# Optimization experiments

Hardware: AMD Instinct MI355X
Metric: run time of the kernel (lower is better)

Reference implementation:

```python
import jax, jax.numpy as jnp
import numpy as np

H = 4      # n_heads
HD = 32    # head_dim
D = 128    # pair channels = H*HD
S = 384    # sequence length
EPS = 1e-5


def setup_inputs() -> dict:
    key = jax.random.key(0)
    ks = jax.random.split(key, 8)
    return {
        "x": jax.random.normal(ks[0], (1, S, S, D), dtype=jnp.float32),
        "attn_mask": jnp.zeros((1, 1, 1, S), dtype=jnp.float32),
        "ln_w": jax.random.uniform(ks[1], (D,), dtype=jnp.float32),
        "ln_b": jax.random.normal(ks[2], (D,), dtype=jnp.float32) * 0.02,
        "bias_w": jax.random.normal(ks[3], (H, D), dtype=jnp.float32) * 0.02,
        "qkv_w": jax.random.normal(ks[4], (3 * H * HD, D), dtype=jnp.float32) * 0.02,
        "g_w": jax.random.normal(ks[5], (H * HD, D), dtype=jnp.float32) * 0.02,
        "o_w": jax.random.normal(ks[6], (D, H * HD), dtype=jnp.float32) * 0.02,
    }


def reference(x, attn_mask, ln_w, ln_b, bias_w, qkv_w, g_w, o_w):
    # x: [1, S, S, D]; ending=False -> no permute
    xs = x[0]  # [S, S, D]; first S = batch of rows, second S = attended axis
    mu = jnp.mean(xs, axis=-1, keepdims=True)
    var = jnp.mean(jnp.square(xs - mu), axis=-1, keepdims=True)
    ln = (xs - mu) * jax.lax.rsqrt(var + EPS) * ln_w + ln_b  # [S, S, D]

    # triangle bias: D -> H, shaped [1, H, S, S], broadcast over row-batch
    bias = jnp.einsum('ijd,hd->hij', ln, bias_w)  # [H, S, S]

    # fused qkv projection, split heads
    qkv = jnp.einsum('bsd,ed->bse', ln, qkv_w)  # [S, S, 3*H*HD]
    q, k, v = jnp.split(qkv, 3, axis=-1)
    def heads(t):
        return t.reshape(S, S, H, HD).transpose(0, 2, 1, 3)  # [S, H, S, HD]
    q, k, v = heads(q), heads(k), heads(v)

    scale = 1.0 / jnp.sqrt(jnp.float32(HD))
    scores = jnp.einsum('bhqd,bhkd->bhqk', q, k) * scale  # [S, H, S, S]
    scores = scores + bias[None] + attn_mask  # attn_mask broadcasts [1,1,1,S]
    attn = jax.nn.softmax(scores, axis=-1)
    o = jnp.einsum('bhqk,bhkd->bhqd', attn, v)  # [S, H, S, HD]
    o = o.transpose(0, 2, 1, 3).reshape(S, S, H * HD)  # concat heads

    g = jnp.einsum('bsd,ed->bse', ln, g_w)  # [S, S, H*HD]
    o = o * jax.nn.sigmoid(g)
    out = jnp.einsum('bse,de->bsd', o, o_w)  # [S, S, D]
    return out[None]  # [1, S, S, D]
```

## Files before the change

### kernel.cpp

```cpp
#include <hip/hip_runtime.h>
#include <hip/hip_bf16.h>


#define S_ 384
#define D_ 128
#define MTOT (S_*S_)

typedef __bf16 bf16;
typedef __bf16 bf16x8 __attribute__((ext_vector_type(8)));
typedef __bf16 bf16x4 __attribute__((ext_vector_type(4)));
typedef float  f32x4  __attribute__((ext_vector_type(4)));

#define LOG2E      1.4426950408889634f
#define QSCALE     0.17677669529663687f
#define QSCALE_L2E 0.25505008455121566f

#if defined(__has_builtin)
#  if __has_builtin(__builtin_amdgcn_exp2f)
#    define HAVE_EXP2 1
#  else
#    define HAVE_EXP2 0
#  endif
#else
#  define HAVE_EXP2 0
#endif

#if HAVE_EXP2
#  define BIAS_MUL LOG2E
#  define Q_MUL    QSCALE_L2E
__device__ __forceinline__ float fast_pexp(float x) { return __builtin_amdgcn_exp2f(x); }
#else
#  define BIAS_MUL 1.0f
#  define Q_MUL    QSCALE
__device__ __forceinline__ float fast_pexp(float x) { return __expf(x); }
#endif

#define OFF_LN   0u
#define OFF_Q    37748736u
#define OFF_K    75497472u
#define OFF_V    113246208u
#define OFF_G    150994944u
#define OFF_BIAS 188743680u
#define OFF_W2   191102976u
#define OFF_OWB  191234048u

__global__ __launch_bounds__(256) void k0_convert(const float* __restrict__ qkv_w,
                                                  const float* __restrict__ g_w,
                                                  const float* __restrict__ o_w,
                                                  bf16* __restrict__ W2,
                                                  bf16* __restrict__ o_wb) {
    int idx = blockIdx.x * 256 + threadIdx.x;
    if (idx < 512 * 128) {
        float v = (idx < 384 * 128) ? qkv_w[idx] : g_w[idx - 384 * 128];
        W2[idx] = (bf16)v;
    }
    int idx2 = idx - 512 * 128;
    if (idx2 >= 0 && idx2 < 128 * 128) o_wb[idx2] = (bf16)o_w[idx2];
}

__global__ __launch_bounds__(256) void k1_ln(const float* __restrict__ x,
                                             const float* __restrict__ ln_w,
                                             const float* __restrict__ ln_b,
                                             const float* __restrict__ bias_w,
                                             const float* __restrict__ mask,
                                             bf16* __restrict__ ln_ws,
                                             float* __restrict__ bias_f) {
    int wid = threadIdx.x >> 6, lane = threadIdx.x & 63;
    int grp = lane >> 5, sub = lane & 31;
    int pos = blockIdx.x * 8 + wid * 2 + grp;
    f32x4 v = ((const f32x4*)(x + (size_t)pos * D_))[sub];
    float sum = v[0] + v[1] + v[2] + v[3];
    float ssq = v[0]*v[0] + v[1]*v[1] + v[2]*v[2] + v[3]*v[3];
    #pragma unroll
    for (int off = 16; off; off >>= 1) {
        sum += __shfl_xor(sum, off);
        ssq += __shfl_xor(ssq, off);
    }
    float mu   = sum * (1.0f / D_);
    float var  = ssq * (1.0f / D_) - mu * mu;
    float rstd = rsqrtf(var + 1e-5f);
    f32x4 w4 = ((const f32x4*)ln_w)[sub];
    f32x4 b4 = ((const f32x4*)ln_b)[sub];
    f32x4 y;
    #pragma unroll
    for (int i = 0; i < 4; ++i) y[i] = (v[i] - mu) * rstd * w4[i] + b4[i];
    bf16x4 yb;
    #pragma unroll
    for (int i = 0; i < 4; ++i) yb[i] = (bf16)y[i];
    *(bf16x4*)(ln_ws + (size_t)pos * D_ + 4 * sub) = yb;

    int ii = pos / S_, jj = pos - ii * S_;
    float mk = mask[jj];
    float p[4];
    #pragma unroll
    for (int h = 0; h < 4; ++h) {
        f32x4 bw = ((const f32x4*)(bias_w + h * D_))[sub];
        p[h] = y[0]*bw[0] + y[1]*bw[1] + y[2]*bw[2] + y[3]*bw[3];
    }
    #pragma unroll
    for (int off = 16; off; off >>= 1)
        #pragma unroll
        for (int h = 0; h < 4; ++h) p[h] += __shfl_xor(p[h], off);
    if (sub == 0) {
        int base = ((ii >> 4) * 24 + (jj >> 4)) * 256 + (((jj >> 2) & 3) * 16 + (ii & 15)) * 4 + (jj & 3);
        #pragma unroll
        for (int h = 0; h < 4; ++h)
            bias_f[h * 147456 + base] = (p[h] + mk) * BIAS_MUL;
    }
}

__global__ __launch_bounds__(512, 2) void k2_proj(const bf16* __restrict__ ln_ws,
                                                  const bf16* __restrict__ W2,
                                                  bf16* __restrict__ q_ws,
                                                  bf16* __restrict__ k_ws,
                                                  bf16* __restrict__ v_ws,
                                                  bf16* __restrict__ g_ws) {
    __shared__ __align__(16) char smem[128 * 272 + 128 * 272];
    char* As = smem;
    char* Bs = smem + 128 * 272;
    char* Cs = smem;
    int t = threadIdx.x;
    int bid = blockIdx.x;
    int xcd = bid & 7;
    int rem = bid >> 3;
    int by  = rem & 3;
    int bx  = ((rem >> 2) << 3) + xcd;
    int m0 = bx * 128;
    int n0 = by * 128;
    #pragma unroll
    for (int it = 0; it < 4; ++it) {
        int byte = it * 8192 + t * 16;
        int row = byte >> 8, colb = byte & 255;
        *(int4*)(As + row * 272 + colb) = *(const int4*)((const char*)ln_ws + (size_t)(m0 + row) * 256 + colb);
    }
    #pragma unroll
    for (int it = 0; it < 4; ++it) {
        int byte = it * 8192 + t * 16;
        int row = byte >> 8, colb = byte & 255;
        *(int4*)(Bs + row * 272 + colb) = *(const int4*)((const char*)W2 + (size_t)(n0 + row) * 256 + colb);
    }
    __syncthreads();
    int wid = t >> 6, lane = t & 63, lr = lane & 15, g = lane >> 4;
    int wm = wid >> 1, wn = wid & 1;
    f32x4 acc[2][4] = {};
    #pragma unroll
    for (int ks = 0; ks < 4; ++ks) {
        bf16x8 af[2], bfr[4];
        #pragma unroll
        for (int mt = 0; mt < 2; ++mt)
            af[mt] = *(const bf16x8*)(As + (wm * 32 + mt * 16 + lr) * 272 + ks * 64 + g * 16);
        #pragma unroll
        for (int nt = 0; nt < 4; ++nt)
            bfr[nt] = *(const bf16x8*)(Bs + (wn * 64 + nt * 16 + lr) * 272 + ks * 64 + g * 16);
        #pragma unroll
        for (int mt = 0; mt < 2; ++mt)
            #pragma unroll
            for (int nt = 0; nt < 4; ++nt)
                acc[mt][nt] = __builtin_amdgcn_mfma_f32_16x16x32_bf16(af[mt], bfr[nt], acc[mt][nt], 0, 0, 0);
    }
    __syncthreads();
    float cmul = (by == 0) ? Q_MUL : 1.0f;
    #pragma unroll
    for (int mt = 0; mt < 2; ++mt)
        #pragma unroll
        for (int nt = 0; nt < 4; ++nt)
            #pragma unroll
            for (int i = 0; i < 4; ++i) {
                int ml = wm * 32 + mt * 16 + g * 4 + i;
                int nl = wn * 64 + nt * 16 + lr;
                *(bf16*)(Cs + ml * 272 + nl * 2) = (bf16)(acc[mt][nt][i] * cmul);
            }
    __syncthreads();
    int b = m0 / 384;
    int jj0 = m0 - b * 384;
    if (by < 2) {
        bf16* dst0 = (by == 0) ? q_ws : k_ws;
        int h = wid >> 1, thalf = wid & 1;
        size_t bh = (size_t)b * 4 + h;
        bf16* dst = dst0 + bh * 12288 + (size_t)((jj0 >> 4) + thalf * 4) * 512 + lane * 8;
        #pragma unroll
        for (int tl = 0; tl < 4; ++tl) {
            bf16x8 v8 = *(const bf16x8*)(Cs + (thalf * 64 + tl * 16 + lr) * 272 + (h * 32 + 8 * g) * 2);
            *(bf16x8*)(dst + tl * 512) = v8;
        }
    } else if (by == 2) {
        int h = wid >> 1, vhalf = wid & 1;
        size_t bh = (size_t)b * 4 + h;
        bf16* dst = v_ws + bh * 12288 + (size_t)(jj0 >> 5) * 1024 + lane * 8;
        #pragma unroll
        for (int f = 0; f < 4; ++f) {
            int kt64 = vhalf * 2 + (f >> 1), dt = f & 1;
            bf16x8 v8;
            #pragma unroll
            for (int j = 0; j < 8; ++j) {
                int kl = 16 * (j >> 2) + 4 * g + (j & 3);
                v8[j] = *(const bf16*)(Cs + (kt64 * 32 + kl) * 272 + (h * 32 + dt * 16 + lr) * 2);
            }
            *(bf16x8*)(dst + kt64 * 1024 + dt * 512) = v8;
        }
    } else {
        #pragma unroll
        for (int j = 0; j < 4; ++j) {
            int byte = j * 8192 + t * 16;
            int ml = byte >> 8, col = byte & 255;
            *(int4*)((char*)g_ws + (size_t)(m0 + ml) * 256 + col) = *(const int4*)(Cs + ml * 272 + col);
        }
    }
}

__global__ __launch_bounds__(512, 6) void k3_attn(const bf16* __restrict__ q_ws,
                                                  const bf16* __restrict__ k_ws,
                                                  const bf16* __restrict__ v_ws,
                                                  const float* __restrict__ bias_f,
                                                  bf16* __restrict__ o_ws) {
    __shared__ __align__(16) char smem[49152];
    char* Ksh = smem;
    char* Vsh = smem + 24576;
    int t = threadIdx.x;
    int bh = blockIdx.x;
    int b = bh >> 2, h = bh & 3;
    const char* kbase = (const char*)(k_ws + (size_t)bh * 12288);
    const char* vbase = (const char*)(v_ws + (size_t)bh * 12288);
    #pragma unroll
    for (int it = 0; it < 3; ++it) {
        int byte = it * 8192 + t * 16;
        *(int4*)(Ksh + byte) = *(const int4*)(kbase + byte);
        *(int4*)(Vsh + byte) = *(const int4*)(vbase + byte);
    }
    __syncthreads();
    int wid = t >> 6, lane = t & 63, lr = lane & 15, g = lane >> 4;
    const char* qbase = (const char*)(q_ws + (size_t)bh * 12288);
    const float* bbase = bias_f + (size_t)h * 147456;
    #pragma unroll 1
    for (int ch = 0; ch < 3; ++ch) {
        int qtile = ch * 8 + wid;
        bf16x8 qf = *(const bf16x8*)(qbase + qtile * 1024 + lane * 16);
        const f32x4* bptr = (const f32x4*)(bbase + qtile * 6144) + lane;
        f32x4 oa[2] = {};
        f32x4 lv = {};
        #pragma unroll 2
        for (int kt = 0; kt < 4; ++kt) {
            bf16x8 pf[3];
            #pragma unroll
            for (int nt = 0; nt < 6; ++nt) {
                int ktile = kt * 6 + nt;
                f32x4 b4 = bptr[ktile * 64];
                bf16x8 kf = *(const bf16x8*)(Ksh + ktile * 1024 + lane * 16);
                f32x4 acc = __builtin_amdgcn_mfma_f32_16x16x32_bf16(kf, qf, b4, 0, 0, 0);
                #pragma unroll
                for (int i = 0; i < 4; ++i) {
                    float p = fast_pexp(acc[i]);
                    lv[i] += p;
                    pf[nt >> 1][(nt & 1) * 4 + i] = (bf16)p;
                }
            }
            #pragma unroll
            for (int tt = 0; tt < 3; ++tt)
                #pragma unroll
                for (int dt = 0; dt < 2; ++dt) {
                    bf16x8 vf = *(const bf16x8*)(Vsh + (kt * 3 + tt) * 2048 + dt * 1024 + lane * 16);
                    oa[dt] = __builtin_amdgcn_mfma_f32_16x16x32_bf16(pf[tt], vf, oa[dt], 0, 0, 0);
                }
        }
        float l = lv[0] + lv[1] + lv[2] + lv[3];
        l += __shfl_xor(l, 16);
        l += __shfl_xor(l, 32);
        float inv = 1.0f / l;
        float invq[4];
        #pragma unroll
        for (int i = 0; i < 4; ++i) invq[i] = __shfl(inv, 4 * g + i);
        int q0 = qtile * 16;
        #pragma unroll
        for (int dt = 0; dt < 2; ++dt)
            #pragma unroll
            for (int i = 0; i < 4; ++i)
                o_ws[((size_t)b * 384 + q0 + 4 * g + i) * 128 + h * 32 + dt * 16 + lr] = (bf16)(oa[dt][i] * invq[i]);
    }
}

__global__ __launch_bounds__(256) void k4_out(const bf16* __restrict__ o_ws,
                                              const bf16* __restrict__ g_ws,
                                              const bf16* __restrict__ o_wb,
                                              float* __restrict__ out) {
    __shared__ __align__(16) char smem[64 * 272 + 128 * 272];
    char* As = smem;
    char* Bs = smem + 64 * 272;
    int t = threadIdx.x;
    int m0 = blockIdx.x * 64;
    #pragma unroll
    for (int it = 0; it < 4; ++it) {
        int byte = it * 4096 + t * 16;
        int row = byte >> 8, colb = byte & 255;
        bf16x8 o8 = *(const bf16x8*)((const char*)o_ws + (size_t)(m0 + row) * 256 + colb);
        bf16x8 g8 = *(const bf16x8*)((const char*)g_ws + (size_t)(m0 + row) * 256 + colb);
        bf16x8 a8;
        #pragma unroll
        for (int j = 0; j < 8; ++j) {
            float ov = (float)o8[j], gv = (float)g8[j];
            a8[j] = (bf16)(ov / (1.0f + __expf(-gv)));
        }
        *(bf16x8*)(As + row * 272 + colb) = a8;
    }
    #pragma unroll
    for (int it = 0; it < 8; ++it) {
        int byte = it * 4096 + t * 16;
        int row = byte >> 8, colb = byte & 255;
        *(int4*)(Bs + row * 272 + colb) = *(const int4*)((const char*)o_wb + (size_t)row * 256 + colb);
    }
    __syncthreads();
    int wid = t >> 6, lane = t & 63, lr = lane & 15, g = lane >> 4;
    int wm = wid >> 1, wn = wid & 1;
    f32x4 acc[2][4] = {};
    #pragma unroll
    for (int ks = 0; ks < 4; ++ks) {
        bf16x8 af[2], bfr[4];
        #pragma unroll
        for (int mt = 0; mt < 2; ++mt)
            af[mt] = *(const bf16x8*)(As + (wm * 32 + mt * 16 + lr) * 272 + ks * 64 + g * 16);
        #pragma unroll
        for (int nt = 0; nt < 4; ++nt)
            bfr[nt] = *(const bf16x8*)(Bs + (wn * 64 + nt * 16 + lr) * 272 + ks * 64 + g * 16);
        #pragma unroll
        for (int mt = 0; mt < 2; ++mt)
            #pragma unroll
            for (int nt = 0; nt < 4; ++nt)
                acc[mt][nt] = __builtin_amdgcn_mfma_f32_16x16x32_bf16(af[mt], bfr[nt], acc[mt][nt], 0, 0, 0);
    }
    #pragma unroll
    for (int mt = 0; mt < 2; ++mt)
        #pragma unroll
        for (int nt = 0; nt < 4; ++nt)
            #pragma unroll
            for (int i = 0; i < 4; ++i) {
                int m = m0 + wm * 32 + mt * 16 + g * 4 + i;
                int n = wn * 64 + nt * 16 + lr;
                out[(size_t)m * 128 + n] = acc[mt][nt][i];
            }
}

extern "C" void kernel_launch(void* const* d_in, const int* in_sizes, int n_in,
                              void* d_out, int out_size, void* d_ws, size_t ws_size,
                              hipStream_t stream) {
    const float* x      = (const float*)d_in[0];
    const float* mask   = (const float*)d_in[1];
    const float* ln_w   = (const float*)d_in[2];
    const float* ln_b   = (const float*)d_in[3];
    const float* bias_w = (const float*)d_in[4];
    const float* qkv_w  = (const float*)d_in[5];
    const float* g_w    = (const float*)d_in[6];
    const float* o_w    = (const float*)d_in[7];
    char* ws = (char*)d_ws;
    bf16*  ln_ws  = (bf16*)(ws + OFF_LN);
    bf16*  q_ws   = (bf16*)(ws + OFF_Q);
    bf16*  k_ws   = (bf16*)(ws + OFF_K);
    bf16*  v_ws   = (bf16*)(ws + OFF_V);
    bf16*  g_ws   = (bf16*)(ws + OFF_G);
    float* bias_f = (float*)(ws + OFF_BIAS);
    bf16*  W2     = (bf16*)(ws + OFF_W2);
    bf16*  o_wb   = (bf16*)(ws + OFF_OWB);
    bf16*  o_ws   = ln_ws;
    float* out    = (float*)d_out;

    k0_convert<<<dim3(320), dim3(256), 0, stream>>>(qkv_w, g_w, o_w, W2, o_wb);
    k1_ln<<<dim3(MTOT / 8), dim3(256), 0, stream>>>(x, ln_w, ln_b, bias_w, mask, ln_ws, bias_f);
    k2_proj<<<dim3(MTOT / 128 * 4), dim3(512), 0, stream>>>(ln_ws, W2, q_ws, k_ws, v_ws, g_ws);
    k3_attn<<<dim3(S_ * 4), dim3(512), 0, stream>>>(q_ws, k_ws, v_ws, bias_f, o_ws);
    k4_out<<<dim3(MTOT / 64), dim3(256), 0, stream>>>(o_ws, g_ws, o_wb, out);
}
```

Before: 179.2 us.

## Process three query tiles per wave in attention and double the output GEMM tile

The attention kernel now keeps three query tiles per wave live simultaneously, so each K and V fragment read from LDS is reused across three MFMA chains instead of being reloaded per chunk. This raises register pressure, so the launch bound drops from 6 to 2 waves-per-EU. The output projection kernel moves to 128-row tiles with 512 threads, which halves how often the o_w weight tile is staged into shared memory per output row. The trade-off is lower occupancy and fewer blocks in the final GEMM.

```diff
diff --git a/kernel.cpp b/kernel.cpp
--- a/kernel.cpp
+++ b/kernel.cpp
@@ -208,7 +208,7 @@
     }
 }
 
-__global__ __launch_bounds__(512, 6) void k3_attn(const bf16* __restrict__ q_ws,
+__global__ __launch_bounds__(512, 2) void k3_attn(const bf16* __restrict__ q_ws,
                                                   const bf16* __restrict__ k_ws,
                                                   const bf16* __restrict__ v_ws,
                                                   const float* __restrict__ bias_f,
@@ -231,65 +231,77 @@
     int wid = t >> 6, lane = t & 63, lr = lane & 15, g = lane >> 4;
     const char* qbase = (const char*)(q_ws + (size_t)bh * 12288);
     const float* bbase = bias_f + (size_t)h * 147456;
+    bf16x8 qf[3];
+    const f32x4* bp[3];
+    #pragma unroll
+    for (int u = 0; u < 3; ++u) {
+        int qtile = wid + u * 8;
+        qf[u] = *(const bf16x8*)(qbase + qtile * 1024 + lane * 16);
+        bp[u] = (const f32x4*)(bbase + qtile * 6144) + lane;
+    }
+    f32x4 oa[3][2] = {};
+    float lsum[3] = {0.f, 0.f, 0.f};
     #pragma unroll 1
-    for (int ch = 0; ch < 3; ++ch) {
-        int qtile = ch * 8 + wid;
-        bf16x8 qf = *(const bf16x8*)(qbase + qtile * 1024 + lane * 16);
-        const f32x4* bptr = (const f32x4*)(bbase + qtile * 6144) + lane;
-        f32x4 oa[2] = {};
-        f32x4 lv = {};
-        #pragma unroll 2
-        for (int kt = 0; kt < 4; ++kt) {
+    for (int kt = 0; kt < 4; ++kt) {
+        #pragma unroll
+        for (int tt = 0; tt < 3; ++tt) {
+            int k0t = kt * 6 + tt * 2;
+            bf16x8 kf0 = *(const bf16x8*)(Ksh + k0t * 1024 + lane * 16);
+            bf16x8 kf1 = *(const bf16x8*)(Ksh + (k0t + 1) * 1024 + lane * 16);
             bf16x8 pf[3];
             #pragma unroll
-            for (int nt = 0; nt < 6; ++nt) {
-                int ktile = kt * 6 + nt;
-                f32x4 b4 = bptr[ktile * 64];
-                bf16x8 kf = *(const bf16x8*)(Ksh + ktile * 1024 + lane * 16);
-                f32x4 acc = __builtin_amdgcn_mfma_f32_16x16x32_bf16(kf, qf, b4, 0, 0, 0);
+            for (int u = 0; u < 3; ++u) {
+                f32x4 a0 = __builtin_amdgcn_mfma_f32_16x16x32_bf16(kf0, qf[u], bp[u][k0t * 64], 0, 0, 0);
+                f32x4 a1 = __builtin_amdgcn_mfma_f32_16x16x32_bf16(kf1, qf[u], bp[u][(k0t + 1) * 64], 0, 0, 0);
                 #pragma unroll
                 for (int i = 0; i < 4; ++i) {
-                    float p = fast_pexp(acc[i]);
-                    lv[i] += p;
-                    pf[nt >> 1][(nt & 1) * 4 + i] = (bf16)p;
+                    float p0 = fast_pexp(a0[i]);
+                    float p1 = fast_pexp(a1[i]);
+                    lsum[u] += p0 + p1;
+                    pf[u][i]     = (bf16)p0;
+                    pf[u][4 + i] = (bf16)p1;
                 }
             }
-            #pragma unroll
-            for (int tt = 0; tt < 3; ++tt)
-                #pragma unroll
-                for (int dt = 0; dt < 2; ++dt) {
-                    bf16x8 vf = *(const bf16x8*)(Vsh + (kt * 3 + tt) * 2048 + dt * 1024 + lane * 16);
-                    oa[dt] = __builtin_amdgcn_mfma_f32_16x16x32_bf16(pf[tt], vf, oa[dt], 0, 0, 0);
-                }
-        }
-        float l = lv[0] + lv[1] + lv[2] + lv[3];
+            const char* vb = Vsh + (kt * 3 + tt) * 2048 + lane * 16;
+            bf16x8 vf0 = *(const bf16x8*)(vb);
+            bf16x8 vf1 = *(const bf16x8*)(vb + 1024);
+            #pragma unroll
+            for (int u = 0; u < 3; ++u) {
+                oa[u][0] = __builtin_amdgcn_mfma_f32_16x16x32_bf16(pf[u], vf0, oa[u][0], 0, 0, 0);
+                oa[u][1] = __builtin_amdgcn_mfma_f32_16x16x32_bf16(pf[u], vf1, oa[u][1], 0, 0, 0);
+            }
+        }
+    }
+    #pragma unroll
+    for (int u = 0; u < 3; ++u) {
+        float l = lsum[u];
         l += __shfl_xor(l, 16);
         l += __shfl_xor(l, 32);
         float inv = 1.0f / l;
         float invq[4];
         #pragma unroll
         for (int i = 0; i < 4; ++i) invq[i] = __shfl(inv, 4 * g + i);
-        int q0 = qtile * 16;
+        int q0 = (wid + u * 8) * 16;
         #pragma unroll
         for (int dt = 0; dt < 2; ++dt)
             #pragma unroll
             for (int i = 0; i < 4; ++i)
-                o_ws[((size_t)b * 384 + q0 + 4 * g + i) * 128 + h * 32 + dt * 16 + lr] = (bf16)(oa[dt][i] * invq[i]);
-    }
-}
-
-__global__ __launch_bounds__(256) void k4_out(const bf16* __restrict__ o_ws,
-                                              const bf16* __restrict__ g_ws,
-                                              const bf16* __restrict__ o_wb,
-                                              float* __restrict__ out) {
-    __shared__ __align__(16) char smem[64 * 272 + 128 * 272];
+                o_ws[((size_t)b * 384 + q0 + 4 * g + i) * 128 + h * 32 + dt * 16 + lr] = (bf16)(oa[u][dt][i] * invq[i]);
+    }
+}
+
+__global__ __launch_bounds__(512, 2) void k4_out(const bf16* __restrict__ o_ws,
+                                                 const bf16* __restrict__ g_ws,
+                                                 const bf16* __restrict__ o_wb,
+                                                 float* __restrict__ out) {
+    __shared__ __align__(16) char smem[128 * 272 + 128 * 272];
     char* As = smem;
-    char* Bs = smem + 64 * 272;
+    char* Bs = smem + 128 * 272;
     int t = threadIdx.x;
-    int m0 = blockIdx.x * 64;
+    int m0 = blockIdx.x * 128;
     #pragma unroll
     for (int it = 0; it < 4; ++it) {
-        int byte = it * 4096 + t * 16;
+        int byte = it * 8192 + t * 16;
         int row = byte >> 8, colb = byte & 255;
         bf16x8 o8 = *(const bf16x8*)((const char*)o_ws + (size_t)(m0 + row) * 256 + colb);
         bf16x8 g8 = *(const bf16x8*)((const char*)g_ws + (size_t)(m0 + row) * 256 + colb);
@@ -302,8 +314,8 @@
         *(bf16x8*)(As + row * 272 + colb) = a8;
     }
     #pragma unroll
-    for (int it = 0; it < 8; ++it) {
-        int byte = it * 4096 + t * 16;
+    for (int it = 0; it < 4; ++it) {
+        int byte = it * 8192 + t * 16;
         int row = byte >> 8, colb = byte & 255;
         *(int4*)(Bs + row * 272 + colb) = *(const int4*)((const char*)o_wb + (size_t)row * 256 + colb);
     }
@@ -365,5 +377,5 @@
     k1_ln<<<dim3(MTOT / 8), dim3(256), 0, stream>>>(x, ln_w, ln_b, bias_w, mask, ln_ws, bias_f);
     k2_proj<<<dim3(MTOT / 128 * 4), dim3(512), 0, stream>>>(ln_ws, W2, q_ws, k_ws, v_ws, g_ws);
     k3_attn<<<dim3(S_ * 4), dim3(512), 0, stream>>>(q_ws, k_ws, v_ws, bias_f, o_ws);
-    k4_out<<<dim3(MTOT / 64), dim3(256), 0, stream>>>(o_ws, g_ws, o_wb, out);
-}
+    k4_out<<<dim3(MTOT / 128), dim3(512), 0, stream>>>(o_ws, g_ws, o_wb, out);
+}
```

Measured after the change: 168.1 us. -6.2%, faster.
